# Performance work log

Measured on AMD Instinct MI355X. Metric: run time of the kernel, lower is better.

## Reference

```python
import jax, jax.numpy as jnp
import numpy as np

MARGIN = 0.1
N = 16384


def setup_inputs() -> dict:
    key = jax.random.key(0)
    k1, k2 = jax.random.split(key)
    pred = jax.random.normal(k1, (N,), dtype=jnp.float32)
    target = jax.random.uniform(k2, (N,), dtype=jnp.float32)
    return {"pred": pred, "target": target}


def reference(pred, target):
    # mask[i, j] = target[j] < target[i]  (the Python loop's Tj per row i)
    mask = target[None, :] < target[:, None]            # [N, N] bool
    # hinge[i, j] = max(0, margin - (pred[i] - pred[j]))
    hinge = jnp.maximum(0.0, MARGIN - (pred[:, None] - pred[None, :]))
    row_sum = jnp.sum(jnp.where(mask, hinge, 0.0), axis=1)   # [N]
    cnt = jnp.sum(mask, axis=1)                               # [N] int
    # rows with no j such that target[j] < target[i] are skipped (continue)
    per_row = jnp.where(cnt > 0, row_sum / jnp.maximum(cnt, 1).astype(pred.dtype), 0.0)
    return jnp.sum(per_row) / pred.shape[0]
```

## Files before the change

### kernel.cpp

```cpp
#include <hip/hip_runtime.h>


constexpr float MARGIN = 0.1f;
constexpr int R = 8;
constexpr int T = 256;

__global__ __launch_bounds__(T) void rank_rows(const float* __restrict__ pred,
                                               const float* __restrict__ target,
                                               float* __restrict__ per_row,
                                               int n) {
    const int base = blockIdx.x * R;

    float ti[R], ci[R];
    #pragma unroll
    for (int r = 0; r < R; ++r) {
        ti[r] = target[base + r];
        ci[r] = MARGIN - pred[base + r];
    }

    float sum[R];
    unsigned int cnt[R];
    #pragma unroll
    for (int r = 0; r < R; ++r) { sum[r] = 0.f; cnt[r] = 0u; }

    const float4* __restrict__ t4 = (const float4*)target;
    const float4* __restrict__ p4 = (const float4*)pred;
    const int n4 = n >> 2;

    for (int j = (int)threadIdx.x; j < n4; j += T) {
        const float4 tj = t4[j];
        const float4 pj = p4[j];
        #pragma unroll
        for (int r = 0; r < R; ++r) {
            const float tir = ti[r], cir = ci[r];
            {
                bool m = tj.x < tir;
                float h = fmaxf(0.f, cir + pj.x);
                sum[r] += m ? h : 0.f;
                cnt[r] += (unsigned)__popcll(__ballot(m));
            }
            {
                bool m = tj.y < tir;
                float h = fmaxf(0.f, cir + pj.y);
                sum[r] += m ? h : 0.f;
                cnt[r] += (unsigned)__popcll(__ballot(m));
            }
            {
                bool m = tj.z < tir;
                float h = fmaxf(0.f, cir + pj.z);
                sum[r] += m ? h : 0.f;
                cnt[r] += (unsigned)__popcll(__ballot(m));
            }
            {
                bool m = tj.w < tir;
                float h = fmaxf(0.f, cir + pj.w);
                sum[r] += m ? h : 0.f;
                cnt[r] += (unsigned)__popcll(__ballot(m));
            }
        }
    }

    __shared__ float        ls[T / 64][R];
    __shared__ unsigned int lc[T / 64][R];
    const int lane = threadIdx.x & 63;
    const int wv   = threadIdx.x >> 6;

    #pragma unroll
    for (int r = 0; r < R; ++r) {
        float s = sum[r];
        #pragma unroll
        for (int off = 32; off > 0; off >>= 1) s += __shfl_down(s, off, 64);
        if (lane == 0) { ls[wv][r] = s; lc[wv][r] = cnt[r]; }
    }
    __syncthreads();

    if ((int)threadIdx.x < R) {
        float s = 0.f;
        unsigned int c = 0u;
        #pragma unroll
        for (int w = 0; w < T / 64; ++w) { s += ls[w][threadIdx.x]; c += lc[w][threadIdx.x]; }
        per_row[base + threadIdx.x] = (c > 0u) ? (s / (float)c) : 0.f;
    }
}

__global__ __launch_bounds__(1024) void final_reduce(const float* __restrict__ per_row,
                                                     float* __restrict__ out, int n) {
    const float4* __restrict__ pr4 = (const float4*)per_row;
    const int n4 = n >> 2;
    double s = 0.0;
    for (int j = (int)threadIdx.x; j < n4; j += 1024) {
        float4 v = pr4[j];
        s += (double)v.x + (double)v.y + (double)v.z + (double)v.w;
    }
    #pragma unroll
    for (int off = 32; off > 0; off >>= 1) s += __shfl_down(s, off, 64);

    __shared__ double sd[16];
    const int lane = threadIdx.x & 63;
    const int wv   = threadIdx.x >> 6;
    if (lane == 0) sd[wv] = s;
    __syncthreads();
    if (threadIdx.x == 0) {
        double t = 0.0;
        #pragma unroll
        for (int w = 0; w < 16; ++w) t += sd[w];
        out[0] = (float)(t / (double)n);
    }
}

extern "C" void kernel_launch(void* const* d_in, const int* in_sizes, int n_in,
                              void* d_out, int out_size, void* d_ws, size_t ws_size,
                              hipStream_t stream) {
    const float* pred   = (const float*)d_in[0];
    const float* target = (const float*)d_in[1];
    const int n = in_sizes[0];

    float* per_row = (float*)d_ws;

    rank_rows<<<n / R, T, 0, stream>>>(pred, target, per_row, n);
    final_reduce<<<1, 1024, 0, stream>>>(per_row, (float*)d_out, n);
}
```

Measured before the change: 90.73 us.

## Bucket-sort by target and compute pairwise hinge only over the lower prefix

```diff
diff --git a/kernel.cpp b/kernel.cpp
--- a/kernel.cpp
+++ b/kernel.cpp
@@ -2,71 +2,139 @@
 
 
 constexpr float MARGIN = 0.1f;
-constexpr int R = 8;
-constexpr int T = 256;
-
-__global__ __launch_bounds__(T) void rank_rows(const float* __restrict__ pred,
-                                               const float* __restrict__ target,
-                                               float* __restrict__ per_row,
-                                               int n) {
-    const int base = blockIdx.x * R;
-
-    float ti[R], ci[R];
-    #pragma unroll
-    for (int r = 0; r < R; ++r) {
-        ti[r] = target[base + r];
-        ci[r] = MARGIN - pred[base + r];
-    }
-
-    float sum[R];
-    unsigned int cnt[R];
-    #pragma unroll
-    for (int r = 0; r < R; ++r) { sum[r] = 0.f; cnt[r] = 0u; }
-
-    const float4* __restrict__ t4 = (const float4*)target;
-    const float4* __restrict__ p4 = (const float4*)pred;
-    const int n4 = n >> 2;
-
-    for (int j = (int)threadIdx.x; j < n4; j += T) {
-        const float4 tj = t4[j];
+constexpr int NBINS  = 4096;
+constexpr int RT     = 16;
+constexpr int T      = 256;
+constexpr int NSLOTS = 256;
+
+__device__ __forceinline__ int bin_of(float t) {
+    int b = (int)(t * (float)NBINS);
+    b = b < 0 ? 0 : b;
+    b = b > NBINS - 1 ? NBINS - 1 : b;
+    return b;
+}
+
+__global__ __launch_bounds__(256) void zero_ws(int* __restrict__ hist,
+                                               float* __restrict__ partials) {
+    int i = blockIdx.x * 256 + (int)threadIdx.x;
+    if (i < NBINS) hist[i] = 0;
+    int j = i - NBINS;
+    if (j >= 0 && j < NSLOTS) partials[j] = 0.f;
+}
+
+__global__ __launch_bounds__(256) void hist_k(const float* __restrict__ target,
+                                              int* __restrict__ hist, int n) {
+    int i = blockIdx.x * 256 + (int)threadIdx.x;
+    if (i < n) atomicAdd(&hist[bin_of(target[i])], 1);
+}
+
+__global__ __launch_bounds__(1024) void scan_k(const int* __restrict__ hist,
+                                               int* __restrict__ B,
+                                               int* __restrict__ cur) {
+    __shared__ int part[1024];
+    const int t = (int)threadIdx.x;
+    int h0 = hist[4 * t + 0], h1 = hist[4 * t + 1];
+    int h2 = hist[4 * t + 2], h3 = hist[4 * t + 3];
+    int tot = h0 + h1 + h2 + h3;
+    part[t] = tot;
+    __syncthreads();
+    for (int off = 1; off < 1024; off <<= 1) {
+        int v = (t >= off) ? part[t - off] : 0;
+        __syncthreads();
+        part[t] += v;
+        __syncthreads();
+    }
+    int excl = part[t] - tot;
+    int b0 = excl, b1 = b0 + h0, b2 = b1 + h1, b3 = b2 + h2;
+    B[4 * t + 0] = b0; B[4 * t + 1] = b1; B[4 * t + 2] = b2; B[4 * t + 3] = b3;
+    cur[4 * t + 0] = b0; cur[4 * t + 1] = b1; cur[4 * t + 2] = b2; cur[4 * t + 3] = b3;
+    if (t == 1023) B[4096] = part[1023];
+}
+
+__global__ __launch_bounds__(256) void scatter_k(const float* __restrict__ pred,
+                                                 const float* __restrict__ target,
+                                                 float* __restrict__ ts,
+                                                 float* __restrict__ ps,
+                                                 int* __restrict__ cur, int n) {
+    int i = blockIdx.x * 256 + (int)threadIdx.x;
+    if (i < n) {
+        float t = target[i], p = pred[i];
+        int pos = atomicAdd(&cur[bin_of(t)], 1);
+        ts[pos] = t;
+        ps[pos] = p;
+    }
+}
+
+__global__ __launch_bounds__(T) void rank_sorted(const float* __restrict__ ts,
+                                                 const float* __restrict__ ps,
+                                                 const int* __restrict__ B,
+                                                 float* __restrict__ partials, int n) {
+    const int g = (int)gridDim.x - 1 - (int)blockIdx.x;
+    const int q = g * RT;
+
+    float ti[RT], ci[RT];
+    #pragma unroll
+    for (int r = 0; r < RT; ++r) {
+        ti[r] = ts[q + r];
+        ci[r] = MARGIN - ps[q + r];
+    }
+
+    const int Blo = B[bin_of(ti[0])];
+    const int Bhi = B[bin_of(ti[RT - 1]) + 1];
+    const int M0 = Blo & ~3;
+    int M1 = (Bhi + 3) & ~3;
+    if (M1 > n) M1 = n;
+
+    float sum[RT];
+    #pragma unroll
+    for (int r = 0; r < RT; ++r) sum[r] = 0.f;
+
+    const float4* __restrict__ p4 = (const float4*)ps;
+    const float4* __restrict__ t4 = (const float4*)ts;
+
+    const int f4 = M0 >> 2;
+    for (int j = (int)threadIdx.x; j < f4; j += T) {
         const float4 pj = p4[j];
         #pragma unroll
-        for (int r = 0; r < R; ++r) {
-            const float tir = ti[r], cir = ci[r];
-            {
-                bool m = tj.x < tir;
-                float h = fmaxf(0.f, cir + pj.x);
-                sum[r] += m ? h : 0.f;
-                cnt[r] += (unsigned)__popcll(__ballot(m));
-            }
-            {
-                bool m = tj.y < tir;
-                float h = fmaxf(0.f, cir + pj.y);
-                sum[r] += m ? h : 0.f;
-                cnt[r] += (unsigned)__popcll(__ballot(m));
-            }
-            {
-                bool m = tj.z < tir;
-                float h = fmaxf(0.f, cir + pj.z);
-                sum[r] += m ? h : 0.f;
-                cnt[r] += (unsigned)__popcll(__ballot(m));
-            }
-            {
-                bool m = tj.w < tir;
-                float h = fmaxf(0.f, cir + pj.w);
-                sum[r] += m ? h : 0.f;
-                cnt[r] += (unsigned)__popcll(__ballot(m));
-            }
+        for (int r = 0; r < RT; ++r) {
+            sum[r] += fmaxf(0.f, ci[r] + pj.x);
+            sum[r] += fmaxf(0.f, ci[r] + pj.y);
+            sum[r] += fmaxf(0.f, ci[r] + pj.z);
+            sum[r] += fmaxf(0.f, ci[r] + pj.w);
         }
     }
 
-    __shared__ float        ls[T / 64][R];
-    __shared__ unsigned int lc[T / 64][R];
-    const int lane = threadIdx.x & 63;
-    const int wv   = threadIdx.x >> 6;
-
-    #pragma unroll
-    for (int r = 0; r < R; ++r) {
+    unsigned int cnt[RT];
+    #pragma unroll
+    for (int r = 0; r < RT; ++r) cnt[r] = 0u;
+
+    const int m4lo = M0 >> 2, m4hi = M1 >> 2;
+    const int iters = (m4hi - m4lo + T - 1) / T;
+    for (int it = 0; it < iters; ++it) {
+        const int j = m4lo + it * T + (int)threadIdx.x;
+        const bool inb = j < m4hi;
+        const int jc = inb ? j : m4lo;
+        const float4 tj = t4[jc];
+        const float4 pj = p4[jc];
+        #pragma unroll
+        for (int r = 0; r < RT; ++r) {
+            { bool m = inb && (tj.x < ti[r]); float h = fmaxf(0.f, ci[r] + pj.x);
+              sum[r] += m ? h : 0.f; cnt[r] += (unsigned)__popcll(__ballot(m)); }
+            { bool m = inb && (tj.y < ti[r]); float h = fmaxf(0.f, ci[r] + pj.y);
+              sum[r] += m ? h : 0.f; cnt[r] += (unsigned)__popcll(__ballot(m)); }
+            { bool m = inb && (tj.z < ti[r]); float h = fmaxf(0.f, ci[r] + pj.z);
+              sum[r] += m ? h : 0.f; cnt[r] += (unsigned)__popcll(__ballot(m)); }
+            { bool m = inb && (tj.w < ti[r]); float h = fmaxf(0.f, ci[r] + pj.w);
+              sum[r] += m ? h : 0.f; cnt[r] += (unsigned)__popcll(__ballot(m)); }
+        }
+    }
+
+    __shared__ float ls[T / 64][RT];
+    __shared__ unsigned int lc[T / 64][RT];
+    const int lane = (int)threadIdx.x & 63;
+    const int wv   = (int)threadIdx.x >> 6;
+    #pragma unroll
+    for (int r = 0; r < RT; ++r) {
         float s = sum[r];
         #pragma unroll
         for (int off = 32; off > 0; off >>= 1) s += __shfl_down(s, off, 64);
@@ -74,37 +142,37 @@
     }
     __syncthreads();
 
-    if ((int)threadIdx.x < R) {
+    __shared__ float vrow[RT];
+    if ((int)threadIdx.x < RT) {
         float s = 0.f;
-        unsigned int c = 0u;
+        unsigned int c = (unsigned int)M0;
         #pragma unroll
         for (int w = 0; w < T / 64; ++w) { s += ls[w][threadIdx.x]; c += lc[w][threadIdx.x]; }
-        per_row[base + threadIdx.x] = (c > 0u) ? (s / (float)c) : 0.f;
-    }
-}
-
-__global__ __launch_bounds__(1024) void final_reduce(const float* __restrict__ per_row,
-                                                     float* __restrict__ out, int n) {
-    const float4* __restrict__ pr4 = (const float4*)per_row;
-    const int n4 = n >> 2;
-    double s = 0.0;
-    for (int j = (int)threadIdx.x; j < n4; j += 1024) {
-        float4 v = pr4[j];
-        s += (double)v.x + (double)v.y + (double)v.z + (double)v.w;
-    }
+        vrow[threadIdx.x] = (c > 0u) ? s / (float)c : 0.f;
+    }
+    __syncthreads();
+    if (threadIdx.x == 0) {
+        float v = 0.f;
+        #pragma unroll
+        for (int r = 0; r < RT; ++r) v += vrow[r];
+        atomicAdd(&partials[blockIdx.x & (NSLOTS - 1)], v);
+    }
+}
+
+__global__ __launch_bounds__(NSLOTS) void final_k(const float* __restrict__ partials,
+                                                  float* __restrict__ out, int n) {
+    float s = partials[threadIdx.x];
     #pragma unroll
     for (int off = 32; off > 0; off >>= 1) s += __shfl_down(s, off, 64);
-
-    __shared__ double sd[16];
-    const int lane = threadIdx.x & 63;
-    const int wv   = threadIdx.x >> 6;
+    __shared__ float sd[NSLOTS / 64];
+    const int lane = (int)threadIdx.x & 63, wv = (int)threadIdx.x >> 6;
     if (lane == 0) sd[wv] = s;
     __syncthreads();
     if (threadIdx.x == 0) {
-        double t = 0.0;
-        #pragma unroll
-        for (int w = 0; w < 16; ++w) t += sd[w];
-        out[0] = (float)(t / (double)n);
+        float t = 0.f;
+        #pragma unroll
+        for (int w = 0; w < NSLOTS / 64; ++w) t += sd[w];
+        out[0] = t / (float)n;
     }
 }
 
@@ -115,8 +183,19 @@
     const float* target = (const float*)d_in[1];
     const int n = in_sizes[0];
 
-    float* per_row = (float*)d_ws;
-
-    rank_rows<<<n / R, T, 0, stream>>>(pred, target, per_row, n);
-    final_reduce<<<1, 1024, 0, stream>>>(per_row, (float*)d_out, n);
-}
+    char* w = (char*)d_ws;
+    size_t o = 0;
+    float* ts       = (float*)(w + o); o += (size_t)n * 4;
+    float* ps       = (float*)(w + o); o += (size_t)n * 4;
+    int*   hist     = (int*)(w + o);   o += (size_t)NBINS * 4;
+    int*   B        = (int*)(w + o);   o += (size_t)(NBINS + 4) * 4;
+    int*   cur      = (int*)(w + o);   o += (size_t)NBINS * 4;
+    float* partials = (float*)(w + o);
+
+    zero_ws<<<(NBINS + NSLOTS + 255) / 256, 256, 0, stream>>>(hist, partials);
+    hist_k<<<(n + 255) / 256, 256, 0, stream>>>(target, hist, n);
+    scan_k<<<1, 1024, 0, stream>>>(hist, B, cur);
+    scatter_k<<<(n + 255) / 256, 256, 0, stream>>>(pred, target, ts, ps, cur, n);
+    rank_sorted<<<n / RT, T, 0, stream>>>(ts, ps, B, partials, n);
+    final_k<<<1, NSLOTS, 0, stream>>>(partials, (float*)d_out, n);
+}
```

Result: faster. 88.71 us (-2.2%).
